# Performance work log

Measured on AMD Instinct MI355X. Metric: run time of the kernel, lower is better.

## Reference

```python
import jax, jax.numpy as jnp
import numpy as np

EPS = 1e-5

def layer_norm(x, w, b):
    m = jnp.mean(x, axis=-1, keepdims=True)
    v = jnp.mean(jnp.square(x - m), axis=-1, keepdims=True)
    return (x - m) * jax.lax.rsqrt(v + EPS) * w + b

def setup_inputs() -> dict:
    key = jax.random.key(0)
    B, S, D, H = 4, 2048, 768, 12
    Dh, F = D // H, 4 * D
    ks = jax.random.split(key, 16)
    s = 0.02
    return {
        "x":    jax.random.normal(ks[0], (B, S, D), dtype=jnp.float32),
        # per-head q/k/v projections stacked over heads: [H, D, Dh]
        "Wq":   jax.random.normal(ks[1], (H, D, Dh), dtype=jnp.float32) * s,
        "bq":   jnp.zeros((H, Dh), dtype=jnp.float32),
        "Wk":   jax.random.normal(ks[2], (H, D, Dh), dtype=jnp.float32) * s,
        "bk":   jnp.zeros((H, Dh), dtype=jnp.float32),
        "Wv":   jax.random.normal(ks[3], (H, D, Dh), dtype=jnp.float32) * s,
        "bv":   jnp.zeros((H, Dh), dtype=jnp.float32),
        "Wo":   jax.random.normal(ks[4], (D, D), dtype=jnp.float32) * s,
        "bo":   jnp.zeros((D,), dtype=jnp.float32),
        "W1":   jax.random.normal(ks[5], (D, F), dtype=jnp.float32) * s,
        "b1":   jnp.zeros((F,), dtype=jnp.float32),
        "W2":   jax.random.normal(ks[6], (F, D), dtype=jnp.float32) * s,
        "b2":   jnp.zeros((D,), dtype=jnp.float32),
        "ln1_w": jnp.ones((D,), dtype=jnp.float32),
        "ln1_b": jnp.zeros((D,), dtype=jnp.float32),
        "ln2_w": jnp.ones((D,), dtype=jnp.float32),
        "ln2_b": jnp.zeros((D,), dtype=jnp.float32),
    }

def reference(x, Wq, bq, Wk, bk, Wv, bv, Wo, bo, W1, b1, W2, b2,
              ln1_w, ln1_b, ln2_w, ln2_b):
    B, S, D = x.shape
    H, _, Dh = Wq.shape
    scale = jnp.sqrt(jnp.float32(Dh))  # torch scales by sqrt(dout)
    # q,k,v: [B, H, S, Dh]
    q = jnp.einsum('bsd,hde->bhse', x, Wq) + bq[None, :, None, :]
    k = jnp.einsum('bsd,hde->bhse', x, Wk) + bk[None, :, None, :]
    v = jnp.einsum('bsd,hde->bhse', x, Wv) + bv[None, :, None, :]
    scores = jnp.einsum('bhqe,bhke->bhqk', q, k) / scale  # [B,H,S,S]
    causal = jnp.tril(jnp.ones((S, S), dtype=bool))
    scores = jnp.where(causal[None, None], scores, -jnp.inf)
    attn = jax.nn.softmax(scores, axis=-1)
    ctx = jnp.einsum('bhqk,bhke->bhqe', attn, v)           # [B,H,S,Dh]
    ctx = jnp.transpose(ctx, (0, 2, 1, 3)).reshape(B, S, D)  # concat heads
    att_out = ctx @ Wo + bo
    h = layer_norm(x + att_out, ln1_w, ln1_b)  # post-norm, dropout=0
    ff = jax.nn.gelu(h @ W1 + b1, approximate=False) @ W2 + b2
    return layer_norm(h + ff, ln2_w, ln2_b)
```

## Files before the change

### kernel.cpp

```cpp
#include <hip/hip_runtime.h>
#include <hip/hip_bf16.h>
#include <math.h>

#define B_ 4
#define S_ 2048
#define D_ 768
#define H_ 12
#define DH_ 64
#define F_ 3072
#define NTOK (B_*S_)
#define BH_ (B_*H_)

typedef __hip_bfloat16 bf16;
typedef __attribute__((ext_vector_type(8))) short bf16x8;
typedef __attribute__((ext_vector_type(4))) float f32x4;
typedef __attribute__((ext_vector_type(4))) _Float16 half4;
typedef __attribute__((ext_vector_type(8))) _Float16 half8;
typedef __attribute__((ext_vector_type(2))) __fp16 fp16x2;

#define GLD16(g, l) __builtin_amdgcn_global_load_lds( \
    (__attribute__((address_space(1))) void*)(uintptr_t)(g), \
    (__attribute__((address_space(3))) void*)(uintptr_t)(l), 16, 0, 0)

__device__ __forceinline__ float bs2f(short s){
  union { unsigned int u; float f; } cv; cv.u = ((unsigned int)(unsigned short)s) << 16; return cv.f;
}
__device__ __forceinline__ float b2f(bf16 v){ return __bfloat162float(v); }
__device__ __forceinline__ bf16 f2b(float v){ return __float2bfloat16(v); }
__device__ __forceinline__ short f2bb(float v){ bf16 b = f2b(v); short s; __builtin_memcpy(&s, &b, 2); return s; }

__device__ __forceinline__ half4 pk4(float p0, float p1, float p2, float p3){
  union { fp16x2 v2[2]; half4 v4; } u;
  u.v2[0] = __builtin_amdgcn_cvt_pkrtz(p0, p1);
  u.v2[1] = __builtin_amdgcn_cvt_pkrtz(p2, p3);
  return u.v4;
}

__device__ __forceinline__ void wgbar(){
  __builtin_amdgcn_s_barrier();
  asm volatile("" ::: "memory");
}
__device__ __forceinline__ void wgbar_lds(){
  asm volatile("s_waitcnt lgkmcnt(0)" ::: "memory");
  __builtin_amdgcn_s_barrier();
  asm volatile("" ::: "memory");
}

__device__ __forceinline__ float gelu_fast(float v){
  const float c0 = -2.302208157f;
  const float c1 = -0.102943238f;
  float w = v*v;
  float z = v * __builtin_fmaf(c1, w, c0);
  float t = __builtin_amdgcn_exp2f(z);
  return v * __builtin_amdgcn_rcpf(1.0f + t);
}

__global__ __launch_bounds__(256) void prep_k(
    const float4* __restrict__ x4, short4* __restrict__ xb4,
    const float* __restrict__ Wo, bf16* __restrict__ WoT,
    const float* __restrict__ W1, bf16* __restrict__ W1T,
    const float* __restrict__ W2, bf16* __restrict__ W2T,
    const float* __restrict__ Wq, const float* __restrict__ bq,
    const float* __restrict__ Wk, const float* __restrict__ bk,
    const float* __restrict__ Wv, const float* __restrict__ bv,
    bf16* __restrict__ Wt, float* __restrict__ bcat)
{
  __shared__ float t[32][33];
  int bid = blockIdx.x;
  const int tidx = threadIdx.x;

  if (bid < 6144){
    const int i = bid*256 + tidx;
    float4 v = x4[i];
    short4 o;
    o.x = f2bb(v.x); o.y = f2bb(v.y); o.z = f2bb(v.z); o.w = f2bb(v.w);
    xb4[i] = o;
    return;
  }
  bid -= 6144;
  if (bid >= 576 + 2304 + 2304){
    bid -= 576 + 2304 + 2304;
    const int idx = bid*256 + tidx;
    {
      int n = idx / D_;
      int k = idx - n*D_;
      int which = n / D_;
      int cc = n - which*D_;
      int h = cc >> 6, e = cc & 63;
      const float* W = (which==0) ? Wq : ((which==1) ? Wk : Wv);
      Wt[idx] = f2b(W[((size_t)h*D_ + k)*DH_ + e]);
    }
    if (idx < 3*D_){
      int which = idx / D_;
      int cc = idx - which*D_;
      int h = cc >> 6, e = cc & 63;
      const float* bb = (which==0) ? bq : ((which==1) ? bk : bv);
      bcat[idx] = bb[h*DH_ + e];
    }
    return;
  }
  const float* tin; bf16* tout; int K, N, tiles_x;
  if (bid < 576){ tin = Wo; tout = WoT; K = D_; N = D_; tiles_x = 24; }
  else if (bid < 576 + 2304){ bid -= 576; tin = W1; tout = W1T; K = D_; N = F_; tiles_x = 96; }
  else { bid -= 576 + 2304; tin = W2; tout = W2T; K = F_; N = D_; tiles_x = 24; }
  const int kb = (bid / tiles_x)*32, nb = (bid % tiles_x)*32;
  const int xx = tidx & 31, y = tidx >> 5;
#pragma unroll
  for (int yy = y; yy < 32; yy += 8)
    t[yy][xx] = tin[(size_t)(kb+yy)*N + nb + xx];
  __syncthreads();
#pragma unroll
  for (int yy = y; yy < 32; yy += 8)
    tout[(size_t)(nb+yy)*K + kb + xx] = f2b(t[xx][yy]);
}

template<int EPI>
__global__ __launch_bounds__(256) void mgemm128_k(
    const bf16* __restrict__ A, const bf16* __restrict__ Bt,
    const float* __restrict__ bias, const bf16* __restrict__ aux,
    bf16* __restrict__ C, int M, int N, int K,
    bf16* __restrict__ qb, bf16* __restrict__ kbuf, _Float16* __restrict__ vt)
{
  __shared__ __align__(16) bf16 As[16384];
  __shared__ __align__(16) bf16 Bs[16384];
  const int tid  = threadIdx.x;
  const int wave = tid >> 6, lane = tid & 63;
  const int quad = lane >> 4, l16 = lane & 15;
  const int wm = (wave >> 1) * 64, wn = (wave & 1) * 64;

  const int NX = gridDim.x;
  const int f  = blockIdx.y * NX + blockIdx.x;
  const int xcd = f & 7;
  const int j   = f >> 3;
  const int bx  = j % NX;
  const int by  = (j / NX) * 8 + xcd;
  const int m0 = by * 128, n0 = bx * 128;

  const int srow8 = lane >> 3;
  const int g     = (lane & 7) ^ srow8;
  const bf16* gA = A  + (size_t)(m0 + wave*32 + srow8)*K + g*8;
  const bf16* gB = Bt + (size_t)(n0 + wave*32 + srow8)*K + g*8;
  const uintptr_t asb = (uintptr_t)(void*)As + (size_t)wave*32*128;
  const uintptr_t bsb = (uintptr_t)(void*)Bs + (size_t)wave*32*128;

  f32x4 acc[4][4];
#pragma unroll
  for (int i=0;i<4;i++)
#pragma unroll
    for (int j2=0;j2<4;j2++) acc[i][j2] = (f32x4)0.f;

  const char* AsB = (const char*)As;
  const char* BsB = (const char*)Bs;
  const int KT = K >> 6;

#pragma unroll
  for (int t=0;t<4;t++){
    GLD16(gA + (size_t)t*8*K, asb + t*1024);
    GLD16(gB + (size_t)t*8*K, bsb + t*1024);
  }
  gA += 64; gB += 64;
  asm volatile("s_waitcnt vmcnt(0)" ::: "memory");
  wgbar();

  for (int kt = 0; kt < KT; ++kt){
    const int cur = kt & 1, nxt = cur ^ 1;
    const bool pf = (kt + 1) < KT;
    if (pf){
      const uintptr_t ao = asb + (size_t)nxt*16384;
      const uintptr_t bo = bsb + (size_t)nxt*16384;
#pragma unroll
      for (int t=0;t<4;t++){
        GLD16(gA + (size_t)t*8*K, ao + t*1024);
        GLD16(gB + (size_t)t*8*K, bo + t*1024);
      }
      gA += 64; gB += 64;
    }
    const char* Ac = AsB + (size_t)cur*16384;
    const char* Bc = BsB + (size_t)cur*16384;
#pragma unroll
    for (int kq = 0; kq < 2; kq++){
      const int cbase = kq*4 + quad;
      bf16x8 af[4], bfr[4];
#pragma unroll
      for (int i=0;i<4;i++){
        const int m = wm + i*16 + l16;
        af[i] = *(const bf16x8*)(Ac + (m << 7) + ((cbase ^ (m & 7)) << 4));
      }
#pragma unroll
      for (int j2=0;j2<4;j2++){
        const int n = wn + j2*16 + l16;
        bfr[j2] = *(const bf16x8*)(Bc + (n << 7) + ((cbase ^ (n & 7)) << 4));
      }
#pragma unroll
      for (int i=0;i<4;i++)
#pragma unroll
        for (int j2=0;j2<4;j2++)
          acc[i][j2] = __builtin_amdgcn_mfma_f32_16x16x32_bf16(af[i], bfr[j2], acc[i][j2], 0, 0, 0);
    }
    if (pf) asm volatile("s_waitcnt vmcnt(0)" ::: "memory");
    wgbar();
  }

#pragma unroll
  for (int i=0;i<4;i++){
#pragma unroll
    for (int j2=0;j2<4;j2++){
      const int n = n0 + wn + j2*16 + l16;
      const int m_base = m0 + wm + i*16 + quad*4;
      if (EPI == 0){
        const int which = n / D_;
        const int cc = n - which*D_;
        const int h = cc >> 6, e = cc & 63;
        if (which == 2){
          const int b = m_base >> 11, s = m_base & (S_-1);
          const int sl = s & 63;
          const int perm = (sl & 32) | (((sl >> 2) & 3) << 3) | ((sl & 16) >> 2);
          half4 hv;
#pragma unroll
          for (int r=0;r<4;r++) hv[r] = (_Float16)(acc[i][j2][r] + bias[n]);
          *(half4*)(vt + ((size_t)(b*H_+h)*DH_ + e)*S_ + (s & ~63) + perm) = hv;
        } else {
          bf16* dst = (which==0) ? qb : kbuf;
          const float sc2 = (which==0) ? 0.18033688f : 1.0f;
#pragma unroll
          for (int r=0;r<4;r++){
            const int m = m_base + r;
            const int b = m >> 11, s = m & (S_-1);
            dst[((size_t)(b*H_+h)*S_ + s)*DH_ + e] = f2b((acc[i][j2][r] + bias[n]) * sc2);
          }
        }
      } else if (EPI == 1){
#pragma unroll
        for (int r=0;r<4;r++){
          const int m = m_base + r;
          float v = acc[i][j2][r] + bias[n] + b2f(aux[(size_t)m*N + n]);
          C[(size_t)m*N + n] = f2b(v);
        }
      } else {
#pragma unroll
        for (int r=0;r<4;r++){
          const int m = m_base + r;
          float v = acc[i][j2][r] + bias[n];
          C[(size_t)m*N + n] = f2b(gelu_fast(v));
        }
      }
    }
  }
}

__global__ __launch_bounds__(512, 4) void fattn_k(const bf16* __restrict__ qb,
    const bf16* __restrict__ kb, const _Float16* __restrict__ vt, bf16* __restrict__ ctx)
{
  __shared__ __align__(16) char smem[36864];
  typedef bf16     KsRow[72];
  typedef _Float16 VsRow[72];
  KsRow* kp0 = (KsRow*)(smem);
  KsRow* kp1 = (KsRow*)(smem + 9216);
  VsRow* vp0 = (VsRow*)(smem + 18432);
  VsRow* vp1 = (VsRow*)(smem + 27648);

  const int bh = blockIdx.x;
  const int qt = 15 - blockIdx.y;
  const int q0 = qt * 128;
  const int tid = threadIdx.x;
  const int wave = tid >> 6, lane = tid & 63;
  const int quad = lane >> 4, l16 = lane & 15;
  const size_t kbase = (size_t)bh * S_ * DH_;
  const int nt = 2*(qt + 1);

  const int sr  = tid >> 3;
  const int seg = (tid & 7) * 8;

  const int qloc = wave*16 + l16;
  const int qglob = q0 + qloc;
  bf16x8 qf[2];
#pragma unroll
  for (int h=0; h<2; h++)
    qf[h] = *(const bf16x8*)(qb + kbase + (size_t)qglob*DH_ + h*32 + quad*8);

  f32x4 o[4];
#pragma unroll
  for (int df=0; df<4; df++) o[df] = (f32x4)0.f;
  float mi = -1e30f, li = 0.f;

  bf16x8 ka; half8 va;
  {
    const bf16* ks = kb + kbase + (size_t)sr*DH_ + seg;
    ka = *(const bf16x8*)ks;
    const _Float16* vs = vt + ((size_t)bh*DH_ + sr)*S_ + seg;
    va = *(const half8*)vs;
  }
  *(bf16x8*)&kp0[sr][seg] = ka;
  *(half8*)&vp0[sr][seg]  = va;
  if (nt > 1){
    ka = *(const bf16x8*)(kb + kbase + (size_t)sr*DH_ + 64*DH_ + seg);
    va = *(const half8*)(vt + ((size_t)bh*DH_ + sr)*S_ + 64 + seg);
  }
  wgbar_lds();

  for (int kt = 0; kt < nt; ++kt){
    const int k0 = kt << 6;
    const bool active = k0 <= q0 + wave*16 + 15;

    f32x4 sc[4];
    half8 vva[4], vvb[4];
    float mx = -1e30f;
    if (active){
#pragma unroll
      for (int mf=0; mf<4; mf++){
        bf16x8 a0 = *(const bf16x8*)&kp0[mf*16 + l16][quad*8];
        bf16x8 a1 = *(const bf16x8*)&kp0[mf*16 + l16][32 + quad*8];
        f32x4 t = __builtin_amdgcn_mfma_f32_16x16x32_bf16(a0, qf[0], (f32x4)0.f, 0, 0, 0);
        sc[mf]  = __builtin_amdgcn_mfma_f32_16x16x32_bf16(a1, qf[1], t, 0, 0, 0);
      }
      if (k0 + 63 > q0 + wave*16){
#pragma unroll
        for (int mf=0; mf<4; mf++){
          const int keyg = k0 + mf*16 + quad*4;
#pragma unroll
          for (int r=0; r<4; r++)
            if (keyg + r > qglob) sc[mf][r] = -1e30f;
        }
      }
#pragma unroll
      for (int mf=0; mf<4; mf++)
#pragma unroll
        for (int r=0; r<4; r++) mx = fmaxf(mx, sc[mf][r]);
      mx = fmaxf(mx, __shfl_xor(mx, 16));
      mx = fmaxf(mx, __shfl_xor(mx, 32));

#pragma unroll
      for (int df=0; df<4; df++){
        vva[df] = *(const half8*)&vp0[df*16 + l16][quad*8];
        vvb[df] = *(const half8*)&vp0[df*16 + l16][32 + quad*8];
      }
    }

    if (kt + 1 < nt){
      *(bf16x8*)&kp1[sr][seg] = ka;
      *(half8*)&vp1[sr][seg]  = va;
      if (kt + 2 < nt){
        const int k0n = (kt + 2) << 6;
        ka = *(const bf16x8*)(kb + kbase + (size_t)(k0n + sr)*DH_ + seg);
        va = *(const half8*)(vt + ((size_t)bh*DH_ + sr)*S_ + k0n + seg);
      }
    }
    wgbar_lds();

    if (active){
      const bool need = !__all(mx - mi <= 8.f);
      if (need){
        const float mn = fmaxf(mi, mx);
        const float a = __builtin_amdgcn_exp2f(mi - mn);
        mi = mn; li *= a;
#pragma unroll
        for (int df=0; df<4; df++)
#pragma unroll
          for (int r=0; r<4; r++) o[df][r] *= a;
      }

      half4 pfr[4];
      float rs = 0.f;
#pragma unroll
      for (int mf=0; mf<4; mf++){
        const float p0 = __builtin_amdgcn_exp2f(sc[mf][0] - mi);
        const float p1 = __builtin_amdgcn_exp2f(sc[mf][1] - mi);
        const float p2 = __builtin_amdgcn_exp2f(sc[mf][2] - mi);
        const float p3 = __builtin_amdgcn_exp2f(sc[mf][3] - mi);
        rs += (p0 + p1) + (p2 + p3);
        pfr[mf] = pk4(p0, p1, p2, p3);
      }
      rs += __shfl_xor(rs, 16);
      rs += __shfl_xor(rs, 32);
      li += rs;

      half8 p01 = __builtin_shufflevector(pfr[0], pfr[1], 0,1,2,3,4,5,6,7);
      half8 p23 = __builtin_shufflevector(pfr[2], pfr[3], 0,1,2,3,4,5,6,7);
#pragma unroll
      for (int df=0; df<4; df++){
        o[df] = __builtin_amdgcn_mfma_f32_16x16x32_f16(vva[df], p01, o[df], 0, 0, 0);
        o[df] = __builtin_amdgcn_mfma_f32_16x16x32_f16(vvb[df], p23, o[df], 0, 0, 0);
      }
    }

    { KsRow* t_ = kp0; kp0 = kp1; kp1 = t_; }
    { VsRow* t_ = vp0; vp0 = vp1; vp1 = t_; }
  }

  const int b = bh / H_, h = bh - (bh / H_)*H_;
  const float inv = 1.0f / li;
  short* cdst = (short*)ctx + ((size_t)(b*S_ + qglob))*D_ + h*DH_;
#pragma unroll
  for (int df=0; df<4; df++){
    short4 pk;
    pk.x = f2bb(o[df][0] * inv);
    pk.y = f2bb(o[df][1] * inv);
    pk.z = f2bb(o[df][2] * inv);
    pk.w = f2bb(o[df][3] * inv);
    *(short4*)(cdst + df*16 + quad*4) = pk;
  }
}

template<typename T> __device__ __forceinline__ void st4(T* p, size_t idx, float a, float b, float c, float d);
template<> __device__ __forceinline__ void st4<float>(float* p, size_t idx, float a, float b, float c, float d){
  float4 v; v.x=a; v.y=b; v.z=c; v.w=d; *(float4*)(p+idx) = v;
}
template<> __device__ __forceinline__ void st4<bf16>(bf16* p, size_t idx, float a, float b, float c, float d){
  short4 v; v.x=f2bb(a); v.y=f2bb(b); v.z=f2bb(c); v.w=f2bb(d); *(short4*)((short*)p+idx) = v;
}

template<typename OutT>
__global__ __launch_bounds__(192) void layernorm_k(const bf16* __restrict__ X,
    const float* __restrict__ g, const float* __restrict__ bta, OutT* __restrict__ Y)
{
  const int row = blockIdx.x;
  const int tid = threadIdx.x;
  const short4 raw = *(const short4*)((const short*)X + (size_t)row*D_ + tid*4);
  const float v0 = bs2f(raw.x), v1 = bs2f(raw.y), v2 = bs2f(raw.z), v3 = bs2f(raw.w);
  float s  = v0+v1+v2+v3;
  float s2 = v0*v0+v1*v1+v2*v2+v3*v3;
#pragma unroll
  for (int o = 32; o > 0; o >>= 1){ s += __shfl_down(s, o); s2 += __shfl_down(s2, o); }
  __shared__ float rs[3], rq[3];
  const int lane = tid & 63, w = tid >> 6;
  if (lane == 0){ rs[w] = s; rq[w] = s2; }
  __syncthreads();
  s  = rs[0]+rs[1]+rs[2];
  s2 = rq[0]+rq[1]+rq[2];
  const float mean = s * (1.0f/D_);
  const float var  = s2 * (1.0f/D_) - mean*mean;
  const float inv  = rsqrtf(var + 1e-5f);
  const float4 g4 = *(const float4*)(g + tid*4);
  const float4 b4 = *(const float4*)(bta + tid*4);
  st4(Y, (size_t)row*D_ + tid*4,
      (v0-mean)*inv*g4.x + b4.x,
      (v1-mean)*inv*g4.y + b4.y,
      (v2-mean)*inv*g4.z + b4.z,
      (v3-mean)*inv*g4.w + b4.w);
}

extern "C" void kernel_launch(void* const* d_in, const int* in_sizes, int n_in,
                              void* d_out, int out_size, void* d_ws, size_t ws_size,
                              hipStream_t stream)
{
  const float* x   = (const float*)d_in[0];
  const float* Wq  = (const float*)d_in[1];
  const float* bq  = (const float*)d_in[2];
  const float* Wk  = (const float*)d_in[3];
  const float* bk  = (const float*)d_in[4];
  const float* Wv  = (const float*)d_in[5];
  const float* bv  = (const float*)d_in[6];
  const float* Wo  = (const float*)d_in[7];
  const float* bo  = (const float*)d_in[8];
  const float* W1  = (const float*)d_in[9];
  const float* b1  = (const float*)d_in[10];
  const float* W2  = (const float*)d_in[11];
  const float* b2  = (const float*)d_in[12];
  const float* g1  = (const float*)d_in[13];
  const float* be1 = (const float*)d_in[14];
  const float* g2  = (const float*)d_in[15];
  const float* be2 = (const float*)d_in[16];
  float* out = (float*)d_out;

  char* ws = (char*)d_ws;
  size_t off = 0;
  auto alloc = [&](size_t bytes)->char*{
    char* p = ws + off; off = (off + bytes + 255) & ~(size_t)255; return p;
  };
  bf16*  xb    = (bf16*) alloc((size_t)NTOK*D_*2);
  bf16*  WcatT = (bf16*) alloc((size_t)3*D_*D_*2);
  float* bcat  = (float*)alloc((size_t)3*D_*4);
  bf16*  WoT   = (bf16*) alloc((size_t)D_*D_*2);
  bf16*  W1T   = (bf16*) alloc((size_t)F_*D_*2);
  bf16*  W2T   = (bf16*) alloc((size_t)D_*F_*2);
  bf16*  r1    = (bf16*) alloc((size_t)NTOK*F_*2);
  bf16*  qb    = r1;
  bf16*  kb    = r1 + (size_t)NTOK*D_;
  _Float16* vt = (_Float16*)(r1 + (size_t)2*NTOK*D_);
  bf16*  ff1   = r1;
  bf16*  ctxb  = (bf16*) alloc((size_t)NTOK*D_*2);
  bf16*  y1    = (bf16*) alloc((size_t)NTOK*D_*2);
  bf16*  hb    = (bf16*) alloc((size_t)NTOK*D_*2);
  bf16*  y2    = ctxb;

  prep_k<<<18240, 256, 0, stream>>>(
      (const float4*)x, (short4*)xb, Wo, WoT, W1, W1T, W2, W2T,
      Wq, bq, Wk, bk, Wv, bv, WcatT, bcat);

  mgemm128_k<0><<<dim3(3*D_/128, NTOK/128), 256, 0, stream>>>(
      xb, WcatT, bcat, nullptr, nullptr, NTOK, 3*D_, D_, qb, kb, vt);

  fattn_k<<<dim3(BH_, S_/128), 512, 0, stream>>>(qb, kb, vt, ctxb);

  mgemm128_k<1><<<dim3(D_/128, NTOK/128), 256, 0, stream>>>(
      ctxb, WoT, bo, xb, y1, NTOK, D_, D_, nullptr, nullptr, nullptr);

  layernorm_k<bf16><<<NTOK, 192, 0, stream>>>(y1, g1, be1, hb);

  mgemm128_k<2><<<dim3(F_/128, NTOK/128), 256, 0, stream>>>(
      hb, W1T, b1, nullptr, ff1, NTOK, F_, D_, nullptr, nullptr, nullptr);

  mgemm128_k<1><<<dim3(D_/128, NTOK/128), 256, 0, stream>>>(
      ff1, W2T, b2, hb, y2, NTOK, D_, F_, nullptr, nullptr, nullptr);

  layernorm_k<float><<<NTOK, 192, 0, stream>>>(y2, g2, be2, out);
}
```

Measured before the change: 359.0 us.

## Shrink attention query tile to 64 with XOR-swizzled unpadded LDS tiles

The flash-attention kernel now uses 64-query tiles with 4 waves (256 threads) instead of 128-query tiles with 8 waves, and launches twice as many blocks. With one 64-key tile per block row, all waves are active every iteration, so the per-wave 'active' check goes away and the causal mask is applied only on the diagonal tile. The padded 72-element LDS rows are replaced by unpadded 128-byte rows with an XOR swizzle to avoid bank conflicts. This cuts wasted work on causal edges and reduces LDS use. The cost is that each loaded K/V tile is reused by fewer queries, so global K/V traffic doubles.

```diff
diff --git a/kernel.cpp b/kernel.cpp
--- a/kernel.cpp
+++ b/kernel.cpp
@@ -248,28 +248,32 @@
   }
 }
 
-__global__ __launch_bounds__(512, 4) void fattn_k(const bf16* __restrict__ qb,
+__global__ __launch_bounds__(256, 4) void fattn_k(const bf16* __restrict__ qb,
     const bf16* __restrict__ kb, const _Float16* __restrict__ vt, bf16* __restrict__ ctx)
 {
-  __shared__ __align__(16) char smem[36864];
-  typedef bf16     KsRow[72];
-  typedef _Float16 VsRow[72];
-  KsRow* kp0 = (KsRow*)(smem);
-  KsRow* kp1 = (KsRow*)(smem + 9216);
-  VsRow* vp0 = (VsRow*)(smem + 18432);
-  VsRow* vp1 = (VsRow*)(smem + 27648);
+  __shared__ __align__(16) char smem[32768];
+  char* kp0 = smem;
+  char* kp1 = smem + 8192;
+  char* vp0 = smem + 16384;
+  char* vp1 = smem + 24576;
 
   const int bh = blockIdx.x;
-  const int qt = 15 - blockIdx.y;
-  const int q0 = qt * 128;
+  const int qt = 31 - blockIdx.y;
+  const int q0 = qt * 64;
   const int tid = threadIdx.x;
   const int wave = tid >> 6, lane = tid & 63;
   const int quad = lane >> 4, l16 = lane & 15;
   const size_t kbase = (size_t)bh * S_ * DH_;
-  const int nt = 2*(qt + 1);
-
-  const int sr  = tid >> 3;
-  const int seg = (tid & 7) * 8;
+  const int nt = qt + 1;
+
+  const int sr = tid >> 2;
+  const int c0 = (tid & 3) * 2;
+  const int w0 = sr*128 + ((c0 ^ (sr & 7)) << 4);
+  const int w1 = sr*128 + (((c0 + 1) ^ (sr & 7)) << 4);
+  const int ge0 = c0*8, ge1 = c0*8 + 8;
+
+  const int sA0 = ((quad       ^ (l16 & 7)) << 4);
+  const int sA1 = (((4 + quad) ^ (l16 & 7)) << 4);
 
   const int qloc = wave*16 + l16;
   const int qglob = q0 + qloc;
@@ -283,108 +287,119 @@
   for (int df=0; df<4; df++) o[df] = (f32x4)0.f;
   float mi = -1e30f, li = 0.f;
 
-  bf16x8 ka; half8 va;
+  bf16x8 ka0, ka1; half8 va0, va1;
   {
-    const bf16* ks = kb + kbase + (size_t)sr*DH_ + seg;
-    ka = *(const bf16x8*)ks;
-    const _Float16* vs = vt + ((size_t)bh*DH_ + sr)*S_ + seg;
-    va = *(const half8*)vs;
-  }
-  *(bf16x8*)&kp0[sr][seg] = ka;
-  *(half8*)&vp0[sr][seg]  = va;
+    const bf16* ks = kb + kbase + (size_t)sr*DH_;
+    ka0 = *(const bf16x8*)(ks + ge0);
+    ka1 = *(const bf16x8*)(ks + ge1);
+    const _Float16* vs = vt + ((size_t)bh*DH_ + sr)*S_;
+    va0 = *(const half8*)(vs + ge0);
+    va1 = *(const half8*)(vs + ge1);
+  }
+  *(bf16x8*)(kp0 + w0) = ka0;
+  *(bf16x8*)(kp0 + w1) = ka1;
+  *(half8*)(vp0 + w0)  = va0;
+  *(half8*)(vp0 + w1)  = va1;
   if (nt > 1){
-    ka = *(const bf16x8*)(kb + kbase + (size_t)sr*DH_ + 64*DH_ + seg);
-    va = *(const half8*)(vt + ((size_t)bh*DH_ + sr)*S_ + 64 + seg);
+    const bf16* ks = kb + kbase + (size_t)(64 + sr)*DH_;
+    ka0 = *(const bf16x8*)(ks + ge0);
+    ka1 = *(const bf16x8*)(ks + ge1);
+    const _Float16* vs = vt + ((size_t)bh*DH_ + sr)*S_ + 64;
+    va0 = *(const half8*)(vs + ge0);
+    va1 = *(const half8*)(vs + ge1);
   }
   wgbar_lds();
 
   for (int kt = 0; kt < nt; ++kt){
-    const int k0 = kt << 6;
-    const bool active = k0 <= q0 + wave*16 + 15;
-
     f32x4 sc[4];
+#pragma unroll
+    for (int mf=0; mf<4; mf++){
+      const int rb = (mf*16 + l16) * 128;
+      bf16x8 a0 = *(const bf16x8*)(kp0 + rb + sA0);
+      bf16x8 a1 = *(const bf16x8*)(kp0 + rb + sA1);
+      f32x4 t = __builtin_amdgcn_mfma_f32_16x16x32_bf16(a0, qf[0], (f32x4)0.f, 0, 0, 0);
+      sc[mf]  = __builtin_amdgcn_mfma_f32_16x16x32_bf16(a1, qf[1], t, 0, 0, 0);
+    }
+
+    if (kt == qt){
+#pragma unroll
+      for (int mf=0; mf<4; mf++){
+        const int keyl = mf*16 + quad*4;
+#pragma unroll
+        for (int r=0; r<4; r++)
+          if (keyl + r > qloc) sc[mf][r] = -1e30f;
+      }
+    }
+
+    float mx = -1e30f;
+#pragma unroll
+    for (int mf=0; mf<4; mf++)
+#pragma unroll
+      for (int r=0; r<4; r++) mx = fmaxf(mx, sc[mf][r]);
+    mx = fmaxf(mx, __shfl_xor(mx, 16));
+    mx = fmaxf(mx, __shfl_xor(mx, 32));
+
     half8 vva[4], vvb[4];
-    float mx = -1e30f;
-    if (active){
-#pragma unroll
-      for (int mf=0; mf<4; mf++){
-        bf16x8 a0 = *(const bf16x8*)&kp0[mf*16 + l16][quad*8];
-        bf16x8 a1 = *(const bf16x8*)&kp0[mf*16 + l16][32 + quad*8];
-        f32x4 t = __builtin_amdgcn_mfma_f32_16x16x32_bf16(a0, qf[0], (f32x4)0.f, 0, 0, 0);
-        sc[mf]  = __builtin_amdgcn_mfma_f32_16x16x32_bf16(a1, qf[1], t, 0, 0, 0);
+#pragma unroll
+    for (int df=0; df<4; df++){
+      const int rb = (df*16 + l16) * 128;
+      vva[df] = *(const half8*)(vp0 + rb + sA0);
+      vvb[df] = *(const half8*)(vp0 + rb + sA1);
+    }
+
+    if (kt + 1 < nt){
+      *(bf16x8*)(kp1 + w0) = ka0;
+      *(bf16x8*)(kp1 + w1) = ka1;
+      *(half8*)(vp1 + w0)  = va0;
+      *(half8*)(vp1 + w1)  = va1;
+      if (kt + 2 < nt){
+        const int k0n = (kt + 2) * 64;
+        const bf16* ks = kb + kbase + (size_t)(k0n + sr)*DH_;
+        ka0 = *(const bf16x8*)(ks + ge0);
+        ka1 = *(const bf16x8*)(ks + ge1);
+        const _Float16* vs = vt + ((size_t)bh*DH_ + sr)*S_ + k0n;
+        va0 = *(const half8*)(vs + ge0);
+        va1 = *(const half8*)(vs + ge1);
       }
-      if (k0 + 63 > q0 + wave*16){
-#pragma unroll
-        for (int mf=0; mf<4; mf++){
-          const int keyg = k0 + mf*16 + quad*4;
-#pragma unroll
-          for (int r=0; r<4; r++)
-            if (keyg + r > qglob) sc[mf][r] = -1e30f;
-        }
-      }
-#pragma unroll
-      for (int mf=0; mf<4; mf++)
-#pragma unroll
-        for (int r=0; r<4; r++) mx = fmaxf(mx, sc[mf][r]);
-      mx = fmaxf(mx, __shfl_xor(mx, 16));
-      mx = fmaxf(mx, __shfl_xor(mx, 32));
-
-#pragma unroll
-      for (int df=0; df<4; df++){
-        vva[df] = *(const half8*)&vp0[df*16 + l16][quad*8];
-        vvb[df] = *(const half8*)&vp0[df*16 + l16][32 + quad*8];
-      }
-    }
-
-    if (kt + 1 < nt){
-      *(bf16x8*)&kp1[sr][seg] = ka;
-      *(half8*)&vp1[sr][seg]  = va;
-      if (kt + 2 < nt){
-        const int k0n = (kt + 2) << 6;
-        ka = *(const bf16x8*)(kb + kbase + (size_t)(k0n + sr)*DH_ + seg);
-        va = *(const half8*)(vt + ((size_t)bh*DH_ + sr)*S_ + k0n + seg);
-      }
     }
     wgbar_lds();
 
-    if (active){
-      const bool need = !__all(mx - mi <= 8.f);
-      if (need){
-        const float mn = fmaxf(mi, mx);
-        const float a = __builtin_amdgcn_exp2f(mi - mn);
-        mi = mn; li *= a;
-#pragma unroll
-        for (int df=0; df<4; df++)
-#pragma unroll
-          for (int r=0; r<4; r++) o[df][r] *= a;
-      }
-
-      half4 pfr[4];
-      float rs = 0.f;
-#pragma unroll
-      for (int mf=0; mf<4; mf++){
-        const float p0 = __builtin_amdgcn_exp2f(sc[mf][0] - mi);
-        const float p1 = __builtin_amdgcn_exp2f(sc[mf][1] - mi);
-        const float p2 = __builtin_amdgcn_exp2f(sc[mf][2] - mi);
-        const float p3 = __builtin_amdgcn_exp2f(sc[mf][3] - mi);
-        rs += (p0 + p1) + (p2 + p3);
-        pfr[mf] = pk4(p0, p1, p2, p3);
-      }
-      rs += __shfl_xor(rs, 16);
-      rs += __shfl_xor(rs, 32);
-      li += rs;
-
-      half8 p01 = __builtin_shufflevector(pfr[0], pfr[1], 0,1,2,3,4,5,6,7);
-      half8 p23 = __builtin_shufflevector(pfr[2], pfr[3], 0,1,2,3,4,5,6,7);
-#pragma unroll
-      for (int df=0; df<4; df++){
-        o[df] = __builtin_amdgcn_mfma_f32_16x16x32_f16(vva[df], p01, o[df], 0, 0, 0);
-        o[df] = __builtin_amdgcn_mfma_f32_16x16x32_f16(vvb[df], p23, o[df], 0, 0, 0);
-      }
-    }
-
-    { KsRow* t_ = kp0; kp0 = kp1; kp1 = t_; }
-    { VsRow* t_ = vp0; vp0 = vp1; vp1 = t_; }
+    const bool need = !__all(mx - mi <= 8.f);
+    if (need){
+      const float mn = fmaxf(mi, mx);
+      const float a = __builtin_amdgcn_exp2f(mi - mn);
+      mi = mn; li *= a;
+#pragma unroll
+      for (int df=0; df<4; df++)
+#pragma unroll
+        for (int r=0; r<4; r++) o[df][r] *= a;
+    }
+
+    half4 pfr[4];
+    float rs = 0.f;
+#pragma unroll
+    for (int mf=0; mf<4; mf++){
+      const float p0 = __builtin_amdgcn_exp2f(sc[mf][0] - mi);
+      const float p1 = __builtin_amdgcn_exp2f(sc[mf][1] - mi);
+      const float p2 = __builtin_amdgcn_exp2f(sc[mf][2] - mi);
+      const float p3 = __builtin_amdgcn_exp2f(sc[mf][3] - mi);
+      rs += (p0 + p1) + (p2 + p3);
+      pfr[mf] = pk4(p0, p1, p2, p3);
+    }
+    rs += __shfl_xor(rs, 16);
+    rs += __shfl_xor(rs, 32);
+    li += rs;
+
+    half8 p01 = __builtin_shufflevector(pfr[0], pfr[1], 0,1,2,3,4,5,6,7);
+    half8 p23 = __builtin_shufflevector(pfr[2], pfr[3], 0,1,2,3,4,5,6,7);
+#pragma unroll
+    for (int df=0; df<4; df++){
+      o[df] = __builtin_amdgcn_mfma_f32_16x16x32_f16(vva[df], p01, o[df], 0, 0, 0);
+      o[df] = __builtin_amdgcn_mfma_f32_16x16x32_f16(vvb[df], p23, o[df], 0, 0, 0);
+    }
+
+    { char* t_ = kp0; kp0 = kp1; kp1 = t_; }
+    { char* t_ = vp0; vp0 = vp1; vp1 = t_; }
   }
 
   const int b = bh / H_, h = bh - (bh / H_)*H_;
@@ -490,7 +505,7 @@
   mgemm128_k<0><<<dim3(3*D_/128, NTOK/128), 256, 0, stream>>>(
       xb, WcatT, bcat, nullptr, nullptr, NTOK, 3*D_, D_, qb, kb, vt);
 
-  fattn_k<<<dim3(BH_, S_/128), 512, 0, stream>>>(qb, kb, vt, ctxb);
+  fattn_k<<<dim3(BH_, S_/64), 256, 0, stream>>>(qb, kb, vt, ctxb);
 
   mgemm128_k<1><<<dim3(D_/128, NTOK/128), 256, 0, stream>>>(
       ctxb, WoT, bo, xb, y1, NTOK, D_, D_, nullptr, nullptr, nullptr);
```

After: 359.0 us. About the same (-0.0%).
